# Kernel optimization log

Hardware: AMD Instinct MI355X
Metric: run time of the kernel (lower is better)

The kernel has to match this reference:

```python
import jax, jax.numpy as jnp
import numpy as np

B, N, DIM, GP = 32, 1024, 768, 49
EPS = 1e-8


def setup_inputs() -> dict:
    key = jax.random.key(0)
    ks = jax.random.split(key, 6)
    s = 1.0 / np.sqrt(DIM)
    return {
        "x": jax.random.normal(ks[0], (B, N, DIM), dtype=jnp.float32),
        "w_qkv": jax.random.normal(ks[1], (DIM, 3 * DIM), dtype=jnp.float32) * s,
        "b_qkv": jnp.zeros((3 * DIM,), dtype=jnp.float32),
        "w_proj": jax.random.normal(ks[2], (DIM, DIM), dtype=jnp.float32) * s,
        "b_proj": jnp.zeros((DIM,), dtype=jnp.float32),
        "w_gp": jax.random.normal(ks[3], (DIM, GP), dtype=jnp.float32) * s,
    }


def reference(x, w_qkv, b_qkv, w_proj, b_proj, w_gp):
    b, n, d = x.shape
    scale = d ** (-0.5)
    qkv = x @ w_qkv + b_qkv                      # [b, n, 3d]
    q, k, v = jnp.split(qkv, 3, axis=-1)          # each [b, n, d]
    # attention scores with softmax over keys
    scores = jnp.einsum("bqd,bkd->bqk", q, k) * scale
    scores = jax.nn.softmax(scores, axis=-1)      # [b, n, n]
    # group-weight modulation: softmax over groups, then outer product
    gw = jax.nn.softmax(v @ w_gp, axis=-1)        # [b, n, gp]
    G = jnp.einsum("bqg,bkg->bqk", gw, gw)        # [b, n, n]
    G = G / (jnp.sum(G, axis=-1, keepdims=True) + EPS) * n
    attn = scores * G
    attn = attn / (jnp.sum(attn, axis=-1, keepdims=True) + EPS)
    out = jnp.einsum("bqk,bkd->bqd", attn, v)     # [b, n, d]
    return out @ w_proj + b_proj
```

## Files before the change

kernel.cpp:

```cpp
#include <hip/hip_runtime.h>
#include <math.h>

typedef short  bf16x8 __attribute__((ext_vector_type(8)));
typedef float  f32x4  __attribute__((ext_vector_type(4)));

__device__ __forceinline__ unsigned short bf16_rn(float x) {
    unsigned u = __float_as_uint(x);
    u += 0x7fffu + ((u >> 16) & 1u);
    return (unsigned short)(u >> 16);
}
__device__ __forceinline__ float bf16f(unsigned short h) {
    return __uint_as_float(((unsigned)h) << 16);
}
__device__ __forceinline__ unsigned fenc(float v) {
    int i = __float_as_int(v);
    return (i >= 0) ? ((unsigned)i | 0x80000000u) : ~((unsigned)i);
}
__device__ __forceinline__ float fdec(unsigned u) {
    int i = (u & 0x80000000u) ? (int)(u & 0x7fffffffu) : ~((int)u);
    return __int_as_float(i);
}

__device__ __forceinline__ void gl2lds16(const void* gptr, void* lptr) {
    __builtin_amdgcn_global_load_lds(
        (const __attribute__((address_space(1))) unsigned int*)(unsigned long long)gptr,
        (__attribute__((address_space(3))) unsigned int*)(unsigned int)(unsigned long long)lptr,
        16, 0, 0);
}

template<int OUTM, bool HAS_BIAS, bool ROWMAX, bool ROWSCALE>
__global__ __launch_bounds__(256, 2)
void mgemm(const unsigned short* __restrict__ Ah_, const unsigned short* __restrict__ Al_,
           const unsigned short* __restrict__ Bh_, const unsigned short* __restrict__ Bl_,
           const float* __restrict__ bias,
           void* o1, void* o2, void* o3, void* o4, void* o5,
           int K, int lda, int ldc,
           long long sA, long long sB, long long sC, float scale)
{
    const int tid = threadIdx.x;
    const int bm = blockIdx.y * 128;
    const int bn = blockIdx.x * 128;
    const long long z = blockIdx.z;

    const unsigned short* Ahu = Ah_ + z * sA;
    const unsigned short* Alu = Al_ + z * sA;
    const unsigned short* Bhu = Bh_ + z * sB;
    const unsigned short* Blu = Bl_ + z * sB;

    __shared__ unsigned short LA_h[2][4096], LA_l[2][4096];
    __shared__ unsigned short LB_h[2][4096], LB_l[2][4096];

    const int wv = tid >> 6, wr = wv >> 1, wc = wv & 1, lane = tid & 63;
    const int fro = (lane >> 4) * 128 + (lane & 15) * 8;

    const int srow = lane & 15, skg = lane >> 4;
    const size_t gaA0 = (size_t)(bm + 16 * wv       + srow) * lda + skg * 8;
    const size_t gaA1 = (size_t)(bm + 16 * (wv + 4) + srow) * lda + skg * 8;
    const size_t gaB0 = (size_t)(bn + 16 * wv       + srow) * lda + skg * 8;
    const size_t gaB1 = (size_t)(bn + 16 * (wv + 4) + srow) * lda + skg * 8;
    const int lo0 = wv * 512, lo1 = (wv + 4) * 512;

    auto stage = [&](int bb, int k0) {
        gl2lds16(&Ahu[gaA0 + k0], &LA_h[bb][lo0]);
        gl2lds16(&Ahu[gaA1 + k0], &LA_h[bb][lo1]);
        gl2lds16(&Alu[gaA0 + k0], &LA_l[bb][lo0]);
        gl2lds16(&Alu[gaA1 + k0], &LA_l[bb][lo1]);
        gl2lds16(&Bhu[gaB0 + k0], &LB_h[bb][lo0]);
        gl2lds16(&Bhu[gaB1 + k0], &LB_h[bb][lo1]);
        gl2lds16(&Blu[gaB0 + k0], &LB_l[bb][lo0]);
        gl2lds16(&Blu[gaB1 + k0], &LB_l[bb][lo1]);
    };

    f32x4 acc[4][4];
#pragma unroll
    for (int i = 0; i < 4; ++i)
#pragma unroll
        for (int j = 0; j < 4; ++j) acc[i][j] = (f32x4){0.f, 0.f, 0.f, 0.f};

    const int nkt = K >> 5;
    stage(0, 0);
    stage(1, 32);
    int cur = 0;
    for (int kt = 0; kt < nkt; ++kt) {
        if (kt < nkt - 1) {
            asm volatile("s_waitcnt vmcnt(8)" ::: "memory");
        } else {
            asm volatile("s_waitcnt vmcnt(0)" ::: "memory");
        }
        __builtin_amdgcn_sched_barrier(0);
        __builtin_amdgcn_s_barrier();
        __builtin_amdgcn_sched_barrier(0);

        bf16x8 bhf[4], blf[4], ahf[4], alf[4];
#pragma unroll
        for (int ni = 0; ni < 4; ++ni) {
            int off = (wc * 4 + ni) * 512 + fro;
            bhf[ni] = *(const bf16x8*)&LB_h[cur][off];
            blf[ni] = *(const bf16x8*)&LB_l[cur][off];
        }
#pragma unroll
        for (int mi = 0; mi < 4; ++mi) {
            int off = (wr * 4 + mi) * 512 + fro;
            ahf[mi] = *(const bf16x8*)&LA_h[cur][off];
            alf[mi] = *(const bf16x8*)&LA_l[cur][off];
        }
        asm volatile("s_waitcnt lgkmcnt(0)" ::: "memory");
        __builtin_amdgcn_sched_barrier(0);
        __builtin_amdgcn_s_barrier();
        __builtin_amdgcn_sched_barrier(0);

        if (kt + 2 < nkt) stage(cur, (kt + 2) << 5);

#pragma unroll
        for (int mi = 0; mi < 4; ++mi) {
#pragma unroll
            for (int ni = 0; ni < 4; ++ni) {
                f32x4 a = acc[mi][ni];
                a = __builtin_amdgcn_mfma_f32_16x16x32_bf16(ahf[mi], bhf[ni], a, 0, 0, 0);
                a = __builtin_amdgcn_mfma_f32_16x16x32_bf16(ahf[mi], blf[ni], a, 0, 0, 0);
                a = __builtin_amdgcn_mfma_f32_16x16x32_bf16(alf[mi], bhf[ni], a, 0, 0, 0);
                acc[mi][ni] = a;
            }
        }
        cur ^= 1;
    }

#pragma unroll
    for (int mi = 0; mi < 4; ++mi) {
#pragma unroll
        for (int ni = 0; ni < 4; ++ni) {
            const int grow0 = bm + wr * 64 + mi * 16 + ((lane >> 4) << 2);
            const int gcol  = bn + wc * 64 + ni * 16 + (lane & 15);
            float bb = HAS_BIAS ? bias[gcol] : 0.f;
#pragma unroll
            for (int r = 0; r < 4; ++r) {
                const int grow = grow0 + r;
                float sc2 = scale;
                if (ROWSCALE) sc2 = ((const float*)o3)[z * 1024 + grow];
                float v = acc[mi][ni][r] * sc2 + bb;
                const size_t growz = (size_t)grow;
                if (OUTM == 0) {
                    ((float*)o1 + z * sC)[growz * ldc + gcol] = v;
                } else if (OUTM == 1) {
                    if (gcol < 768) {
                        unsigned short h = bf16_rn(v);
                        ((unsigned short*)o1)[growz * 768 + gcol] = h;
                        ((unsigned short*)o2)[growz * 768 + gcol] = bf16_rn(v - bf16f(h));
                    } else if (gcol < 1536) {
                        int cc = gcol - 768;
                        unsigned short h = bf16_rn(v);
                        ((unsigned short*)o3)[growz * 768 + cc] = h;
                        ((unsigned short*)o4)[growz * 768 + cc] = bf16_rn(v - bf16f(h));
                    } else {
                        ((float*)o5)[growz * 768 + (gcol - 1536)] = v;
                    }
                } else {
                    unsigned short h = bf16_rn(v);
                    ((unsigned short*)o1 + z * sC)[growz * ldc + gcol] = h;
                    ((unsigned short*)o2 + z * sC)[growz * ldc + gcol] = bf16_rn(v - bf16f(h));
                }
            }
        }
    }

    if (OUTM == 0 && ROWMAX) {
        unsigned* mrow = (unsigned*)o2 + z * 1024;
#pragma unroll
        for (int mi = 0; mi < 4; ++mi) {
            const int grow0 = bm + wr * 64 + mi * 16 + ((lane >> 4) << 2);
#pragma unroll
            for (int r = 0; r < 4; ++r) {
                float mx = acc[mi][0][r];
#pragma unroll
                for (int ni = 1; ni < 4; ++ni) mx = fmaxf(mx, acc[mi][ni][r]);
                mx *= scale;
#pragma unroll
                for (int off = 1; off < 16; off <<= 1)
                    mx = fmaxf(mx, __shfl_xor(mx, off));
                if ((lane & 15) == 0) atomicMax(&mrow[grow0 + r], fenc(mx));
            }
        }
    }
}

__global__ __launch_bounds__(256)
void split_k(const float* __restrict__ src, unsigned short* __restrict__ dh,
             unsigned short* __restrict__ dl, long long n8)
{
    long long i = (long long)blockIdx.x * 256 + threadIdx.x;
    const long long stride = (long long)gridDim.x * 256;
    for (; i < n8; i += stride) {
        const float4* p = (const float4*)(src + i * 8);
        float4 f0 = p[0], f1 = p[1];
        float ff[8] = {f0.x, f0.y, f0.z, f0.w, f1.x, f1.y, f1.z, f1.w};
        bf16x8 hv, lv;
#pragma unroll
        for (int j = 0; j < 8; ++j) {
            unsigned short h = bf16_rn(ff[j]);
            hv[j] = (short)h;
            lv[j] = (short)bf16_rn(ff[j] - bf16f(h));
        }
        *(bf16x8*)(dh + i * 8) = hv;
        *(bf16x8*)(dl + i * 8) = lv;
    }
}

__global__ __launch_bounds__(256)
void tsplit_k(const float* __restrict__ src, unsigned short* __restrict__ dh,
              unsigned short* __restrict__ dl, int ls, long long ss,
              int ld_, long long sd)
{
    src += (long long)blockIdx.z * ss;
    dh  += (long long)blockIdx.z * sd;
    dl  += (long long)blockIdx.z * sd;
    __shared__ float t[32][33];
    const int tx = threadIdx.x & 31, ty = threadIdx.x >> 5;
    const int r0 = blockIdx.y * 32, c0 = blockIdx.x * 32;
#pragma unroll
    for (int i = 0; i < 4; ++i)
        t[ty + 8 * i][tx] = src[(size_t)(r0 + ty + 8 * i) * ls + c0 + tx];
    __syncthreads();
#pragma unroll
    for (int i = 0; i < 4; ++i) {
        float v = t[tx][ty + 8 * i];
        unsigned short h = bf16_rn(v);
        size_t o = (size_t)(c0 + ty + 8 * i) * ld_ + r0 + tx;
        dh[o] = h;
        dl[o] = bf16_rn(v - bf16f(h));
    }
}

__global__ __launch_bounds__(64)
void gw_k(const float* __restrict__ Vf, const float* __restrict__ wgp,
          unsigned short* __restrict__ gh, unsigned short* __restrict__ gl)
{
    const long long row = blockIdx.x;
    const int lane = threadIdx.x;
    const float* v = Vf + row * 768;
    float a0 = 0.f, a1 = 0.f, a2 = 0.f, a3 = 0.f;
    if (lane < 49) {
        for (int d = 0; d < 768; d += 4) {
            float4 vv = *(const float4*)&v[d];
            a0 = fmaf(vv.x, wgp[(d + 0) * 49 + lane], a0);
            a1 = fmaf(vv.y, wgp[(d + 1) * 49 + lane], a1);
            a2 = fmaf(vv.z, wgp[(d + 2) * 49 + lane], a2);
            a3 = fmaf(vv.w, wgp[(d + 3) * 49 + lane], a3);
        }
    }
    float logit = (lane < 49) ? ((a0 + a1) + (a2 + a3)) : -INFINITY;
    float m = logit;
    for (int off = 32; off; off >>= 1) m = fmaxf(m, __shfl_xor(m, off));
    float e = (lane < 49) ? expf(logit - m) : 0.f;
    float s = e;
    for (int off = 32; off; off >>= 1) s += __shfl_xor(s, off);
    float val = e / s;
    unsigned short h = bf16_rn(val);
    gh[row * 64 + lane] = h;
    gl[row * 64 + lane] = bf16_rn(val - bf16f(h));
}

__global__ __launch_bounds__(256)
void minit_k(unsigned* __restrict__ m, int n)
{
    int i = blockIdx.x * 256 + threadIdx.x;
    if (i < n) m[i] = 0x007FFFFFu;
}

__global__ __launch_bounds__(256, 2)
void modm_k(const float* __restrict__ SC,
            const unsigned short* __restrict__ gwH, const unsigned short* __restrict__ gwL,
            const unsigned* __restrict__ menc,
            float* __restrict__ fvec,
            unsigned short* __restrict__ Sh, unsigned short* __restrict__ Sl)
{
    const int tid = threadIdx.x;
    const int qb  = blockIdx.x;
    const long long b = blockIdx.y;
    const int wv = tid >> 6, wr = wv >> 1, wc = wv & 1, lane = tid & 63;
    const int l15 = lane & 15, l4 = lane >> 4;

    const long long rowblk = b * 1024 + qb * 64;

    bf16x8 ah[2][2], al[2][2];
#pragma unroll
    for (int mi = 0; mi < 2; ++mi)
#pragma unroll
        for (int kt = 0; kt < 2; ++kt) {
            long long ga = (rowblk + wr * 32 + mi * 16 + l15) * 64 + kt * 32 + l4 * 8;
            ah[mi][kt] = *(const bf16x8*)&gwH[ga];
            al[mi][kt] = *(const bf16x8*)&gwL[ga];
        }

    float mval[8];
#pragma unroll
    for (int mi = 0; mi < 2; ++mi)
#pragma unroll
        for (int r = 0; r < 4; ++r) {
            long long row = rowblk + wr * 32 + mi * 16 + l4 * 4 + r;
            mval[mi * 4 + r] = fdec(menc[row]);
        }

    float Tp[8], Zp[8], Gp[8];
#pragma unroll
    for (int s = 0; s < 8; ++s) { Tp[s] = 0.f; Zp[s] = 0.f; Gp[s] = 0.f; }

    for (int kn = 0; kn < 8; ++kn) {
        bf16x8 bh[4][2], bl[4][2];
#pragma unroll
        for (int ni = 0; ni < 4; ++ni)
#pragma unroll
            for (int kt = 0; kt < 2; ++kt) {
                long long gb = (b * 1024 + kn * 128 + wc * 64 + ni * 16 + l15) * 64
                             + kt * 32 + l4 * 8;
                bh[ni][kt] = *(const bf16x8*)&gwH[gb];
                bl[ni][kt] = *(const bf16x8*)&gwL[gb];
            }
#pragma unroll
        for (int mi = 0; mi < 2; ++mi) {
            f32x4 acc[4];
#pragma unroll
            for (int ni = 0; ni < 4; ++ni) {
                f32x4 a = (f32x4){0.f, 0.f, 0.f, 0.f};
#pragma unroll
                for (int kt = 0; kt < 2; ++kt) {
                    a = __builtin_amdgcn_mfma_f32_16x16x32_bf16(ah[mi][kt], bh[ni][kt], a, 0, 0, 0);
                    a = __builtin_amdgcn_mfma_f32_16x16x32_bf16(ah[mi][kt], bl[ni][kt], a, 0, 0, 0);
                    a = __builtin_amdgcn_mfma_f32_16x16x32_bf16(al[mi][kt], bh[ni][kt], a, 0, 0, 0);
                }
                acc[ni] = a;
            }
#pragma unroll
            for (int ni = 0; ni < 4; ++ni) {
                const int col = kn * 128 + wc * 64 + ni * 16 + l15;
#pragma unroll
                for (int r = 0; r < 4; ++r) {
                    const long long row = rowblk + wr * 32 + mi * 16 + l4 * 4 + r;
                    float s = SC[row * 1024 + col];
                    float e = expf(s - mval[mi * 4 + r]);
                    float g = acc[ni][r];
                    float w = e * g;
                    Tp[mi * 4 + r] += w;
                    Zp[mi * 4 + r] += e;
                    Gp[mi * 4 + r] += g;
                    unsigned short h = bf16_rn(w);
                    Sh[row * 1024 + col] = h;
                    Sl[row * 1024 + col] = bf16_rn(w - bf16f(h));
                }
            }
        }
    }
#pragma unroll
    for (int s = 0; s < 8; ++s) {
#pragma unroll
        for (int off = 1; off < 16; off <<= 1) {
            Tp[s] += __shfl_xor(Tp[s], off);
            Zp[s] += __shfl_xor(Zp[s], off);
            Gp[s] += __shfl_xor(Gp[s], off);
        }
    }
    __shared__ float red[2][64][4];
    if (l15 == 0) {
#pragma unroll
        for (int mi = 0; mi < 2; ++mi)
#pragma unroll
            for (int r = 0; r < 4; ++r) {
                int rl = wr * 32 + mi * 16 + l4 * 4 + r;
                red[wc][rl][0] = Tp[mi * 4 + r];
                red[wc][rl][1] = Zp[mi * 4 + r];
                red[wc][rl][2] = Gp[mi * 4 + r];
            }
    }
    __syncthreads();
    if (tid < 64) {
        float T  = red[0][tid][0] + red[1][tid][0];
        float Z  = red[0][tid][1] + red[1][tid][1];
        float SG = red[0][tid][2] + red[1][tid][2];
        float c = 1024.f / (Z * (SG + 1e-8f));
        float f = c / (c * T + 1e-8f);
        fvec[rowblk + tid] = f;
    }
}

extern "C" void kernel_launch(void* const* d_in, const int* in_sizes, int n_in,
                              void* d_out, int out_size, void* d_ws, size_t ws_size,
                              hipStream_t stream)
{
    const float* x      = (const float*)d_in[0];
    const float* w_qkv  = (const float*)d_in[1];
    const float* b_qkv  = (const float*)d_in[2];
    const float* w_proj = (const float*)d_in[3];
    const float* b_proj = (const float*)d_in[4];
    const float* w_gp   = (const float*)d_in[5];
    float* out = (float*)d_out;

    auto need = [](int CB) -> size_t {
        size_t u = 0;
        u += 2ull * 2304 * 768;
        u += 2ull * 768 * 768;
        u += 4ull * CB * 1024 * 768;
        u += 2ull * CB * 1024 * 768;
        u += 2ull * CB * 1024 * 1024;
        u += 2ull * CB * 1024 * 64;
        size_t bytes = u * 2;
        bytes += 4ull * ((size_t)CB * 1024 * 768
                       + (size_t)CB * 1024 * 1024
                       + (size_t)CB * 1024
                       + (size_t)CB * 1024);
        return bytes + 8192;
    };
    int CB = 32;
    while (CB > 1 && need(CB) > ws_size) CB >>= 1;
    const int MC = CB * 1024;

    char* cur = (char*)d_ws;
    auto alloc_u = [&](size_t n) {
        unsigned short* p = (unsigned short*)cur;
        cur += ((n * 2 + 15) & ~15ull);
        return p;
    };
    auto alloc_f = [&](size_t n) {
        float* p = (float*)cur;
        cur += ((n * 4 + 15) & ~15ull);
        return p;
    };
    unsigned short* WqTh = alloc_u(2304ull * 768);
    unsigned short* WqTl = alloc_u(2304ull * 768);
    unsigned short* WpTh = alloc_u(768ull * 768);
    unsigned short* WpTl = alloc_u(768ull * 768);
    unsigned short* Qh   = alloc_u((size_t)MC * 768);
    unsigned short* Ql   = alloc_u((size_t)MC * 768);
    unsigned short* Kh   = alloc_u((size_t)MC * 768);
    unsigned short* Kl   = alloc_u((size_t)MC * 768);
    unsigned short* VTh  = alloc_u((size_t)MC * 768);
    unsigned short* VTl  = alloc_u((size_t)MC * 768);
    unsigned short* Sh   = alloc_u((size_t)MC * 1024);
    unsigned short* Sl   = alloc_u((size_t)MC * 1024);
    unsigned short* gwH  = alloc_u((size_t)MC * 64);
    unsigned short* gwL  = alloc_u((size_t)MC * 64);
    float* Vf   = alloc_f((size_t)MC * 768);
    float* SC   = alloc_f((size_t)MC * 1024);
    float* fvec = alloc_f((size_t)MC);
    unsigned* menc = (unsigned*)alloc_f((size_t)MC);
    unsigned short* Oh = Qh;
    unsigned short* Ol = Ql;
    unsigned short* Xh = Sh;
    unsigned short* Xl = Sl;

    const float scale = 1.0f / sqrtf(768.0f);

    tsplit_k<<<dim3(72, 24, 1), 256, 0, stream>>>(w_qkv, WqTh, WqTl, 2304, 0, 768, 0);
    tsplit_k<<<dim3(24, 24, 1), 256, 0, stream>>>(w_proj, WpTh, WpTl, 768, 0, 768, 0);

    for (int c = 0; c < 32 / CB; ++c) {
        const float* xc   = x   + (size_t)c * MC * 768;
        float*       outc = out + (size_t)c * MC * 768;

        {
            const long long n8 = (long long)MC * 768 / 8;
            int nb = (int)((n8 + 255) / 256);
            if (nb > 4096) nb = 4096;
            split_k<<<dim3(nb), 256, 0, stream>>>(xc, Xh, Xl, n8);
        }

        mgemm<1, true, false, false><<<dim3(18, MC / 128, 1), 256, 0, stream>>>(
            Xh, Xl, WqTh, WqTl, b_qkv,
            Qh, Ql, Kh, Kl, Vf, 768, 768, 0, 0, 0, 0, 1.0f);

        gw_k<<<dim3(MC), 64, 0, stream>>>(Vf, w_gp, gwH, gwL);

        tsplit_k<<<dim3(24, 32, CB), 256, 0, stream>>>(
            Vf, VTh, VTl, 768, 1024ll * 768, 1024, 768ll * 1024);

        minit_k<<<dim3((MC + 255) / 256), 256, 0, stream>>>(menc, MC);

        mgemm<0, false, true, false><<<dim3(8, 8, CB), 256, 0, stream>>>(
            Qh, Ql, Kh, Kl, nullptr,
            SC, menc, nullptr, nullptr, nullptr,
            768, 768, 1024, 1024ll * 768, 1024ll * 768, 1024ll * 1024, scale);

        modm_k<<<dim3(16, CB), 256, 0, stream>>>(SC, gwH, gwL, menc, fvec, Sh, Sl);

        mgemm<2, false, false, true><<<dim3(6, 8, CB), 256, 0, stream>>>(
            Sh, Sl, VTh, VTl, nullptr,
            Oh, Ol, fvec, nullptr, nullptr,
            1024, 1024, 768, 1024ll * 1024, 768ll * 1024, 1024ll * 768, 1.0f);

        mgemm<0, true, false, false><<<dim3(6, MC / 128, 1), 256, 0, stream>>>(
            Oh, Ol, WpTh, WpTl, b_proj,
            outc, nullptr, nullptr, nullptr, nullptr,
            768, 768, 768, 0, 0, 0, 1.0f);
    }
}
```

Measured before the change: 1.610 ms.

## Widen GEMM tiles to 128x256 with 8 waves and triple-buffered LDS pipeline

The split-bf16 MFMA GEMM now uses 512 threads (8 waves) per block and a 128x256 output tile, halving the grid in the N dimension. The LDS ring goes from two to three stages, so the next prefetch can be issued right after the top barrier, and the second per-iteration barrier is removed. MFMA sections are wrapped in s_setprio to favour math issue. LDS use rises to about 144 KB per block, which likely limits residency to one block per CU, and the smaller grids cut parallelism for the small GEMMs.

```diff
diff --git a/kernel.cpp b/kernel.cpp
--- a/kernel.cpp
+++ b/kernel.cpp
@@ -29,7 +29,7 @@
 }
 
 template<int OUTM, bool HAS_BIAS, bool ROWMAX, bool ROWSCALE>
-__global__ __launch_bounds__(256, 2)
+__global__ __launch_bounds__(512, 2)
 void mgemm(const unsigned short* __restrict__ Ah_, const unsigned short* __restrict__ Al_,
            const unsigned short* __restrict__ Bh_, const unsigned short* __restrict__ Bl_,
            const float* __restrict__ bias,
@@ -39,7 +39,7 @@
 {
     const int tid = threadIdx.x;
     const int bm = blockIdx.y * 128;
-    const int bn = blockIdx.x * 128;
+    const int bn = blockIdx.x * 256;
     const long long z = blockIdx.z;
 
     const unsigned short* Ahu = Ah_ + z * sA;
@@ -47,28 +47,26 @@
     const unsigned short* Bhu = Bh_ + z * sB;
     const unsigned short* Blu = Bl_ + z * sB;
 
-    __shared__ unsigned short LA_h[2][4096], LA_l[2][4096];
-    __shared__ unsigned short LB_h[2][4096], LB_l[2][4096];
-
-    const int wv = tid >> 6, wr = wv >> 1, wc = wv & 1, lane = tid & 63;
+    __shared__ unsigned short LA_h[3][4096], LA_l[3][4096];
+    __shared__ unsigned short LB_h[3][8192], LB_l[3][8192];
+
+    const int wv = tid >> 6, lane = tid & 63;
+    const int wr = wv >> 2, wc = wv & 3;
     const int fro = (lane >> 4) * 128 + (lane & 15) * 8;
 
     const int srow = lane & 15, skg = lane >> 4;
-    const size_t gaA0 = (size_t)(bm + 16 * wv       + srow) * lda + skg * 8;
-    const size_t gaA1 = (size_t)(bm + 16 * (wv + 4) + srow) * lda + skg * 8;
-    const size_t gaB0 = (size_t)(bn + 16 * wv       + srow) * lda + skg * 8;
-    const size_t gaB1 = (size_t)(bn + 16 * (wv + 4) + srow) * lda + skg * 8;
-    const int lo0 = wv * 512, lo1 = (wv + 4) * 512;
+    const size_t gaA  = (size_t)(bm + 16 * wv + srow) * lda + skg * 8;
+    const size_t gaB0 = (size_t)(bn + 32 * wv + srow) * lda + skg * 8;
+    const size_t gaB1 = (size_t)(bn + 32 * wv + 16 + srow) * lda + skg * 8;
+    const int loA = wv * 512, loB = wv * 1024;
 
     auto stage = [&](int bb, int k0) {
-        gl2lds16(&Ahu[gaA0 + k0], &LA_h[bb][lo0]);
-        gl2lds16(&Ahu[gaA1 + k0], &LA_h[bb][lo1]);
-        gl2lds16(&Alu[gaA0 + k0], &LA_l[bb][lo0]);
-        gl2lds16(&Alu[gaA1 + k0], &LA_l[bb][lo1]);
-        gl2lds16(&Bhu[gaB0 + k0], &LB_h[bb][lo0]);
-        gl2lds16(&Bhu[gaB1 + k0], &LB_h[bb][lo1]);
-        gl2lds16(&Blu[gaB0 + k0], &LB_l[bb][lo0]);
-        gl2lds16(&Blu[gaB1 + k0], &LB_l[bb][lo1]);
+        gl2lds16(&Ahu[gaA  + k0], &LA_h[bb][loA]);
+        gl2lds16(&Alu[gaA  + k0], &LA_l[bb][loA]);
+        gl2lds16(&Bhu[gaB0 + k0], &LB_h[bb][loB]);
+        gl2lds16(&Bhu[gaB1 + k0], &LB_h[bb][loB + 512]);
+        gl2lds16(&Blu[gaB0 + k0], &LB_l[bb][loB]);
+        gl2lds16(&Blu[gaB1 + k0], &LB_l[bb][loB + 512]);
     };
 
     f32x4 acc[4][4];
@@ -80,10 +78,10 @@
     const int nkt = K >> 5;
     stage(0, 0);
     stage(1, 32);
-    int cur = 0;
     for (int kt = 0; kt < nkt; ++kt) {
+        const int cb = kt % 3;
         if (kt < nkt - 1) {
-            asm volatile("s_waitcnt vmcnt(8)" ::: "memory");
+            asm volatile("s_waitcnt vmcnt(6)" ::: "memory");
         } else {
             asm volatile("s_waitcnt vmcnt(0)" ::: "memory");
         }
@@ -91,26 +89,25 @@
         __builtin_amdgcn_s_barrier();
         __builtin_amdgcn_sched_barrier(0);
 
+        if (kt + 2 < nkt) stage((kt + 2) % 3, (kt + 2) << 5);
+
         bf16x8 bhf[4], blf[4], ahf[4], alf[4];
 #pragma unroll
         for (int ni = 0; ni < 4; ++ni) {
             int off = (wc * 4 + ni) * 512 + fro;
-            bhf[ni] = *(const bf16x8*)&LB_h[cur][off];
-            blf[ni] = *(const bf16x8*)&LB_l[cur][off];
+            bhf[ni] = *(const bf16x8*)&LB_h[cb][off];
+            blf[ni] = *(const bf16x8*)&LB_l[cb][off];
         }
 #pragma unroll
         for (int mi = 0; mi < 4; ++mi) {
             int off = (wr * 4 + mi) * 512 + fro;
-            ahf[mi] = *(const bf16x8*)&LA_h[cur][off];
-            alf[mi] = *(const bf16x8*)&LA_l[cur][off];
+            ahf[mi] = *(const bf16x8*)&LA_h[cb][off];
+            alf[mi] = *(const bf16x8*)&LA_l[cb][off];
         }
         asm volatile("s_waitcnt lgkmcnt(0)" ::: "memory");
         __builtin_amdgcn_sched_barrier(0);
-        __builtin_amdgcn_s_barrier();
-        __builtin_amdgcn_sched_barrier(0);
-
-        if (kt + 2 < nkt) stage(cur, (kt + 2) << 5);
-
+
+        __builtin_amdgcn_s_setprio(1);
 #pragma unroll
         for (int mi = 0; mi < 4; ++mi) {
 #pragma unroll
@@ -122,7 +119,7 @@
                 acc[mi][ni] = a;
             }
         }
-        cur ^= 1;
+        __builtin_amdgcn_s_setprio(0);
     }
 
 #pragma unroll
@@ -462,7 +459,7 @@
             split_k<<<dim3(nb), 256, 0, stream>>>(xc, Xh, Xl, n8);
         }
 
-        mgemm<1, true, false, false><<<dim3(18, MC / 128, 1), 256, 0, stream>>>(
+        mgemm<1, true, false, false><<<dim3(9, MC / 128, 1), 512, 0, stream>>>(
             Xh, Xl, WqTh, WqTl, b_qkv,
             Qh, Ql, Kh, Kl, Vf, 768, 768, 0, 0, 0, 0, 1.0f);
 
@@ -473,19 +470,19 @@
 
         minit_k<<<dim3((MC + 255) / 256), 256, 0, stream>>>(menc, MC);
 
-        mgemm<0, false, true, false><<<dim3(8, 8, CB), 256, 0, stream>>>(
+        mgemm<0, false, true, false><<<dim3(4, 8, CB), 512, 0, stream>>>(
             Qh, Ql, Kh, Kl, nullptr,
             SC, menc, nullptr, nullptr, nullptr,
             768, 768, 1024, 1024ll * 768, 1024ll * 768, 1024ll * 1024, scale);
 
         modm_k<<<dim3(16, CB), 256, 0, stream>>>(SC, gwH, gwL, menc, fvec, Sh, Sl);
 
-        mgemm<2, false, false, true><<<dim3(6, 8, CB), 256, 0, stream>>>(
+        mgemm<2, false, false, true><<<dim3(3, 8, CB), 512, 0, stream>>>(
             Sh, Sl, VTh, VTl, nullptr,
             Oh, Ol, fvec, nullptr, nullptr,
             1024, 1024, 768, 1024ll * 1024, 768ll * 1024, 1024ll * 768, 1.0f);
 
-        mgemm<0, true, false, false><<<dim3(6, MC / 128, 1), 256, 0, stream>>>(
+        mgemm<0, true, false, false><<<dim3(3, MC / 128, 1), 512, 0, stream>>>(
             Oh, Ol, WpTh, WpTl, b_proj,
             outc, nullptr, nullptr, nullptr, nullptr,
             768, 768, 768, 0, 0, 0, 1.0f);
```

Result: faster. 1.569 ms (-2.5%).
